# Performance work log

Measured on AMD Instinct MI355X. Metric: run time of the kernel, lower is better.

The kernel has to match this reference:

```python
import jax, jax.numpy as jnp
import numpy as np

H = 1024       # hidden_size
V = 32000      # output_vocab_size
STEPS = 375    # fixed greedy decode length in the original loop


def setup_inputs() -> dict:
    key = jax.random.key(0)
    ks = jax.random.split(key, 6)
    s = 0.02  # init scale
    return {
        "encoder_hidden": jax.random.normal(ks[0], (1, 1, H), dtype=jnp.float32),
        "emb": jax.random.normal(ks[1], (V, H), dtype=jnp.float32) * s,
        "W_ih": jax.random.normal(ks[2], (3 * H, H), dtype=jnp.float32) * s,   # [W_ir;W_iz;W_in]
        "W_hh": jax.random.normal(ks[3], (3 * H, H), dtype=jnp.float32) * s,   # [W_hr;W_hz;W_hn]
        "b_ih": jnp.zeros((3 * H,), dtype=jnp.float32),
        "b_hh": jnp.zeros((3 * H,), dtype=jnp.float32),
        "lin_W": jax.random.normal(ks[4], (V, H), dtype=jnp.float32) * s,
        "lin_b": jnp.zeros((V,), dtype=jnp.float32),
    }


def _gru_cell(x, h, W_ih, W_hh, b_ih, b_hh):
    # PyTorch GRU gate math (gate order r, z, n)
    gi = W_ih @ x + b_ih            # [3H]
    gh = W_hh @ h + b_hh            # [3H]
    i_r, i_z, i_n = jnp.split(gi, 3)
    h_r, h_z, h_n = jnp.split(gh, 3)
    r = jax.nn.sigmoid(i_r + h_r)
    z = jax.nn.sigmoid(i_z + h_z)
    n = jnp.tanh(i_n + r * h_n)
    return (1.0 - z) * n + z * h


def reference(encoder_hidden, emb, W_ih, W_hh, b_ih, b_hh, lin_W, lin_b):
    h0 = encoder_hidden[0, 0]  # [H], batch=1, single layer

    def step(carry, _):
        h, tok = carry
        x = emb[tok]                                   # embedding lookup [H]
        h_new = _gru_cell(x, h, W_ih, W_hh, b_ih, b_hh)
        logits = lin_W @ h_new + lin_b                 # [V]
        logp = jax.nn.log_softmax(logits)              # LogSoftmax(dim=1) on [1,V]
        next_tok = jnp.argmax(logp).astype(jnp.int32)  # greedy feedback
        return (h_new, next_tok), logp

    (h_final, _), outs = jax.lax.scan(
        step, (h0, jnp.int32(0)), None, length=STEPS)
    # original cats [1,V] outputs along dim 0 -> [STEPS, V]
    return outs, h_final.reshape(1, 1, H)
```

## Files before the change

### kernel.cpp

```cpp
#include <hip/hip_runtime.h>

#define H 1024
#define V 32000
#define STEPS 375
#define NB1 256
#define NB2 512
#define DELTA 0.0625f

__device__ __forceinline__ float dot4(const float4 a, const float4 b) {
    return fmaf(a.x, b.x, fmaf(a.y, b.y, fmaf(a.z, b.z, a.w * b.w)));
}

__device__ __forceinline__ float wave_sum(float v) {
#pragma unroll
    for (int off = 32; off > 0; off >>= 1) v += __shfl_xor(v, off);
    return v;
}

__device__ __forceinline__ void sm_merge(float& m, float& ss, int& a,
                                         float om, float os, int oa) {
    if (om > m || (om == m && oa < a)) {
        ss = os + ss * expf(m - om); m = om; a = oa;
    } else {
        ss += os * expf(om - m);
    }
}

__device__ __forceinline__ float bl(unsigned u) { return __uint_as_float(u << 16); }
__device__ __forceinline__ float bh(unsigned u) { return __uint_as_float(u & 0xffff0000u); }

__device__ __forceinline__ unsigned f2bf(float f) {
    unsigned u = __float_as_uint(f);
    return (u + 0x7fffu + ((u >> 16) & 1u)) >> 16;
}

__global__ void init_kernel(const float* __restrict__ enc, float* __restrict__ h0) {
    for (int i = threadIdx.x; i < H; i += 256) h0[i] = enc[i];
}

__global__ __launch_bounds__(512) void conv_kernel(const float* __restrict__ src,
                                                   unsigned short* __restrict__ dst) {
    const size_t idx = (size_t)blockIdx.x * 512 + threadIdx.x;
    const float4* s4 = (const float4*)src;
    float4 a = s4[2 * idx], b = s4[2 * idx + 1];
    uint4 o;
    o.x = f2bf(a.x) | (f2bf(a.y) << 16);
    o.y = f2bf(a.z) | (f2bf(a.w) << 16);
    o.z = f2bf(b.x) | (f2bf(b.y) << 16);
    o.w = f2bf(b.z) | (f2bf(b.w) << 16);
    ((uint4*)dst)[idx] = o;
}

__global__ __launch_bounds__(256) void gru_kernel(
    const float* __restrict__ emb, const float* __restrict__ W_ih,
    const float* __restrict__ W_hh, const float* __restrict__ b_ih,
    const float* __restrict__ b_hh, const float* __restrict__ h_cur,
    float* __restrict__ h_next, float* __restrict__ logz,
    const float* __restrict__ pm, const float* __restrict__ ps,
    const int* __restrict__ pa, int s) {
    const int tid = threadIdx.x;
    const int lane = tid & 63;
    const int wv = tid >> 6;
    const int b = blockIdx.x;
    const int i = b * 4 + wv;

    const float4* hp = (const float4*)h_cur;
    float4 hv[4];
    float4 WX0[4], WX1[4], WX2[4], WH0[4], WH1[4], WH2[4];
#pragma unroll
    for (int j = 0; j < 4; ++j) {
        const int idx = lane + 64 * j;
        hv[j] = hp[idx];
        WX0[j] = ((const float4*)(W_ih + (size_t)i * H))[idx];
        WX1[j] = ((const float4*)(W_ih + ((size_t)i + H) * H))[idx];
        WX2[j] = ((const float4*)(W_ih + ((size_t)i + 2 * H) * H))[idx];
        WH0[j] = ((const float4*)(W_hh + (size_t)i * H))[idx];
        WH1[j] = ((const float4*)(W_hh + ((size_t)i + H) * H))[idx];
        WH2[j] = ((const float4*)(W_hh + ((size_t)i + 2 * H) * H))[idx];
    }

    int tok = 0;
    if (s > 0) {
        float m = -3.4e38f, ss = 0.f;
        int a = 0x7fffffff;
#pragma unroll
        for (int k = 0; k < NB2 / 64; ++k)
            sm_merge(m, ss, a, pm[k * 64 + lane], ps[k * 64 + lane], pa[k * 64 + lane]);
#pragma unroll
        for (int off = 32; off > 0; off >>= 1) {
            float om = __shfl_xor(m, off), os = __shfl_xor(ss, off);
            int oa = __shfl_xor(a, off);
            sm_merge(m, ss, a, om, os, oa);
        }
        tok = a;
        if (b == 0 && tid == 0) logz[s - 1] = m + logf(ss);
    }

    const float4* xp = (const float4*)(emb + (size_t)tok * H);
    float4 xv[4];
#pragma unroll
    for (int j = 0; j < 4; ++j) xv[j] = xp[lane + 64 * j];

    float sx0 = 0, sx1 = 0, sx2 = 0, sh0 = 0, sh1 = 0, sh2 = 0;
#pragma unroll
    for (int j = 0; j < 4; ++j) {
        sx0 += dot4(WX0[j], xv[j]); sx1 += dot4(WX1[j], xv[j]); sx2 += dot4(WX2[j], xv[j]);
        sh0 += dot4(WH0[j], hv[j]); sh1 += dot4(WH1[j], hv[j]); sh2 += dot4(WH2[j], hv[j]);
    }
    sx0 = wave_sum(sx0); sx1 = wave_sum(sx1); sx2 = wave_sum(sx2);
    sh0 = wave_sum(sh0); sh1 = wave_sum(sh1); sh2 = wave_sum(sh2);
    if (lane == 0) {
        const float rg = 1.f / (1.f + expf(-((sx0 + b_ih[i]) + (sh0 + b_hh[i]))));
        const float zg = 1.f / (1.f + expf(-((sx1 + b_ih[i + H]) + (sh1 + b_hh[i + H]))));
        const float ng = tanhf((sx2 + b_ih[i + 2 * H]) + rg * (sh2 + b_hh[i + 2 * H]));
        h_next[i] = (1.f - zg) * ng + zg * h_cur[i];
    }
}

__global__ __launch_bounds__(512, 4) void logits_bf16_kernel(
    const unsigned short* __restrict__ wbf, const float* __restrict__ lin_W,
    const float* __restrict__ lin_b, const float* __restrict__ h_src,
    float* __restrict__ orow, float* __restrict__ pm, float* __restrict__ ps,
    int* __restrict__ pa) {
    const int tid = threadIdx.x;
    const int lane = tid & 63;
    const int wv = tid >> 6;
    const int b = blockIdx.x;
    const int row0 = (b < 256) ? 63 * b : 16128 + 62 * (b - 256);
    const int nrows = (b < 256) ? 63 : 62;

    __shared__ float red_m[8], red_s[8];
    __shared__ float s_cm[8];
    __shared__ int s_ca[8];

    const float4* h4 = (const float4*)h_src;
    const float4 ha0 = h4[2 * lane], ha1 = h4[2 * lane + 1];
    const float4 hb0 = h4[128 + 2 * lane], hb1 = h4[129 + 2 * lane];
    const float h0[8] = {ha0.x, ha0.y, ha0.z, ha0.w, ha1.x, ha1.y, ha1.z, ha1.w};
    const float h1[8] = {hb0.x, hb0.y, hb0.z, hb0.w, hb1.x, hb1.y, hb1.z, hb1.w};

    uint4 qa[8], qb[8];
    bool val[8];
#pragma unroll
    for (int k = 0; k < 8; ++k) {
        const int rr = wv + 8 * k;
        val[k] = rr < nrows;
        const uint4* wp = (const uint4*)(wbf + (size_t)(row0 + (val[k] ? rr : 0)) * H);
        qa[k] = wp[lane];
        qb[k] = wp[64 + lane];
    }
    __builtin_amdgcn_sched_barrier(0);

    float lg[8];
    float m = -3.4e38f, ssum = 0.f;
#pragma unroll
    for (int k = 0; k < 8; ++k) {
        float a = 0.f;
        a = fmaf(bl(qa[k].x), h0[0], a); a = fmaf(bh(qa[k].x), h0[1], a);
        a = fmaf(bl(qa[k].y), h0[2], a); a = fmaf(bh(qa[k].y), h0[3], a);
        a = fmaf(bl(qa[k].z), h0[4], a); a = fmaf(bh(qa[k].z), h0[5], a);
        a = fmaf(bl(qa[k].w), h0[6], a); a = fmaf(bh(qa[k].w), h0[7], a);
        a = fmaf(bl(qb[k].x), h1[0], a); a = fmaf(bh(qb[k].x), h1[1], a);
        a = fmaf(bl(qb[k].y), h1[2], a); a = fmaf(bh(qb[k].y), h1[3], a);
        a = fmaf(bl(qb[k].z), h1[4], a); a = fmaf(bh(qb[k].z), h1[5], a);
        a = fmaf(bl(qb[k].w), h1[6], a); a = fmaf(bh(qb[k].w), h1[7], a);
        a = wave_sum(a);
        if (val[k]) {
            const int col = row0 + wv + 8 * k;
            a += lin_b[col];
            lg[k] = a;
            if (lane == 0) __builtin_nontemporal_store(a, &orow[col]);
            if (a > m) { ssum *= expf(m - a); m = a; }
            ssum += expf(a - m);
        } else {
            lg[k] = -3.4e38f;
        }
    }
    if (lane == 0) { red_m[wv] = m; red_s[wv] = ssum; }
    __syncthreads();

    float Mb = red_m[0];
#pragma unroll
    for (int w = 1; w < 8; ++w) Mb = fmaxf(Mb, red_m[w]);

    float cm = -3.4e38f;
    int ca = 0x7fffffff;
    float4 hv[4];
    bool loaded = false;
#pragma unroll
    for (int k = 0; k < 8; ++k) {
        if (lg[k] > Mb - DELTA) {
            const int row = row0 + wv + 8 * k;
            if (!loaded) {
#pragma unroll
                for (int j = 0; j < 4; ++j) hv[j] = h4[lane + 64 * j];
                loaded = true;
            }
            const float4* rp = (const float4*)(lin_W + (size_t)row * H);
            float a = 0.f;
#pragma unroll
            for (int j = 0; j < 4; ++j) a += dot4(rp[lane + 64 * j], hv[j]);
            a = wave_sum(a) + lin_b[row];
            if (a > cm || (a == cm && row < ca)) { cm = a; ca = row; }
        }
    }
    if (lane == 0) { s_cm[wv] = cm; s_ca[wv] = ca; }
    __syncthreads();
    if (tid == 0) {
        float M = red_m[0], S = red_s[0];
#pragma unroll
        for (int w = 1; w < 8; ++w) {
            const float mw = red_m[w], sw = red_s[w];
            if (mw > M) { S = sw + S * expf(M - mw); M = mw; }
            else S += sw * expf(mw - M);
        }
        float CM = s_cm[0];
        int CA = s_ca[0];
#pragma unroll
        for (int w = 1; w < 8; ++w)
            if (s_cm[w] > CM || (s_cm[w] == CM && s_ca[w] < CA)) { CM = s_cm[w]; CA = s_ca[w]; }
        pm[b] = CM;
        ps[b] = S * expf(M - CM);
        pa[b] = CA;
    }
}

__global__ __launch_bounds__(512, 4) void logits_fp32_kernel(
    const float* __restrict__ lin_W, const float* __restrict__ lin_b,
    const float* __restrict__ h_src, float* __restrict__ orow,
    float* __restrict__ pm, float* __restrict__ ps, int* __restrict__ pa) {
    const int tid = threadIdx.x;
    const int lane = tid & 63;
    const int wv = tid >> 6;
    const int b = blockIdx.x;
    const int row0 = (b < 256) ? 63 * b : 16128 + 62 * (b - 256);
    const int nrows = (b < 256) ? 63 : 62;

    __shared__ float red_m[8], red_s[8];
    __shared__ int red_a[8];

    const float4* h4 = (const float4*)h_src;
    float4 hr[4];
#pragma unroll
    for (int j = 0; j < 4; ++j) hr[j] = h4[lane + 64 * j];

    float m = -3.4e38f, ssum = 0.f;
    int arg = 0x7fffffff;
    for (int r = wv; r < nrows; r += 32) {
        const int rB = r + 8, rC = r + 16, rD = r + 24;
        const bool vB = rB < nrows, vC = rC < nrows, vD = rD < nrows;
        float4 wA[4], wB[4], wC[4], wD[4];
#pragma unroll
        for (int j = 0; j < 4; ++j) {
            const int idx = lane + 64 * j;
            wA[j] = ((const float4*)(lin_W + (size_t)(row0 + r) * H))[idx];
            wB[j] = ((const float4*)(lin_W + (size_t)(row0 + (vB ? rB : r)) * H))[idx];
            wC[j] = ((const float4*)(lin_W + (size_t)(row0 + (vC ? rC : r)) * H))[idx];
            wD[j] = ((const float4*)(lin_W + (size_t)(row0 + (vD ? rD : r)) * H))[idx];
        }
        __builtin_amdgcn_sched_barrier(0);
        float aA = 0, aB = 0, aC = 0, aD = 0;
#pragma unroll
        for (int j = 0; j < 4; ++j) {
            aA += dot4(wA[j], hr[j]); aB += dot4(wB[j], hr[j]);
            aC += dot4(wC[j], hr[j]); aD += dot4(wD[j], hr[j]);
        }
        aA = wave_sum(aA); aB = wave_sum(aB);
        aC = wave_sum(aC); aD = wave_sum(aD);
        aA += lin_b[row0 + r];
        if (lane == 0) __builtin_nontemporal_store(aA, &orow[row0 + r]);
        if (aA > m) { ssum *= expf(m - aA); m = aA; arg = row0 + r; }
        ssum += expf(aA - m);
        if (vB) {
            aB += lin_b[row0 + rB];
            if (lane == 0) __builtin_nontemporal_store(aB, &orow[row0 + rB]);
            if (aB > m) { ssum *= expf(m - aB); m = aB; arg = row0 + rB; }
            ssum += expf(aB - m);
        }
        if (vC) {
            aC += lin_b[row0 + rC];
            if (lane == 0) __builtin_nontemporal_store(aC, &orow[row0 + rC]);
            if (aC > m) { ssum *= expf(m - aC); m = aC; arg = row0 + rC; }
            ssum += expf(aC - m);
        }
        if (vD) {
            aD += lin_b[row0 + rD];
            if (lane == 0) __builtin_nontemporal_store(aD, &orow[row0 + rD]);
            if (aD > m) { ssum *= expf(m - aD); m = aD; arg = row0 + rD; }
            ssum += expf(aD - m);
        }
    }
    if (lane == 0) { red_m[wv] = m; red_s[wv] = ssum; red_a[wv] = arg; }
    __syncthreads();
    if (tid == 0) {
        float M = red_m[0], S = red_s[0];
        int A = red_a[0];
#pragma unroll
        for (int w = 1; w < 8; ++w) sm_merge(M, S, A, red_m[w], red_s[w], red_a[w]);
        pm[b] = M; ps[b] = S; pa[b] = A;
    }
}

__global__ __launch_bounds__(256) void final_kernel(float* __restrict__ out,
                                                    const float* __restrict__ logz) {
    const int row = blockIdx.x >> 3;
    const int seg = blockIdx.x & 7;
    const float lz = logz[row];
    float4* p = (float4*)(out + (size_t)row * V) + seg * 1000;
    for (int i = threadIdx.x; i < 1000; i += 256) {
        float4 v = p[i];
        v.x -= lz; v.y -= lz; v.z -= lz; v.w -= lz;
        p[i] = v;
    }
}

__global__ __launch_bounds__(256) void tail_kernel(
    float* __restrict__ out_last, const float* __restrict__ pm,
    const float* __restrict__ ps, const int* __restrict__ pa,
    const float* __restrict__ h_final, float* __restrict__ out_h) {
    const int tid = threadIdx.x;
    const int lane = tid & 63;
    const int b = blockIdx.x;
    float m = -3.4e38f, ss = 0.f;
    int a = 0x7fffffff;
#pragma unroll
    for (int k = 0; k < NB2 / 64; ++k)
        sm_merge(m, ss, a, pm[k * 64 + lane], ps[k * 64 + lane], pa[k * 64 + lane]);
#pragma unroll
    for (int off = 32; off > 0; off >>= 1) {
        float om = __shfl_xor(m, off), os = __shfl_xor(ss, off);
        int oa = __shfl_xor(a, off);
        sm_merge(m, ss, a, om, os, oa);
    }
    const float logZ = m + logf(ss);
    if (tid < 125) out_last[b * 125 + tid] -= logZ;
    if (b == 0)
        for (int i = tid; i < H; i += 256) out_h[i] = h_final[i];
}

extern "C" void kernel_launch(void* const* d_in, const int* in_sizes, int n_in,
                              void* d_out, int out_size, void* d_ws, size_t ws_size,
                              hipStream_t stream) {
    const float* enc = (const float*)d_in[0];
    const float* emb = (const float*)d_in[1];
    const float* W_ih = (const float*)d_in[2];
    const float* W_hh = (const float*)d_in[3];
    const float* b_ih = (const float*)d_in[4];
    const float* b_hh = (const float*)d_in[5];
    const float* lin_W = (const float*)d_in[6];
    const float* lin_b = (const float*)d_in[7];
    float* out = (float*)d_out;
    float* ws = (float*)d_ws;

    float* h_buf = ws;
    float* pm = ws + 2 * H;
    float* ps = pm + NB2;
    int* pa = (int*)(ps + NB2);
    float* logz = (float*)(pa + NB2);
    unsigned short* wbf = (unsigned short*)((char*)d_ws + 16384);
    const size_t need = 16384 + (size_t)V * H * 2;
    const bool bf16path = ws_size >= need;

    init_kernel<<<1, 256, 0, stream>>>(enc, h_buf);
    if (bf16path)
        conv_kernel<<<V * H / 8 / 512, 512, 0, stream>>>(lin_W, wbf);
    for (int s = 0; s < STEPS; ++s) {
        float* h_cur = h_buf + (s & 1) * H;
        float* h_next = h_buf + ((s + 1) & 1) * H;
        gru_kernel<<<NB1, 256, 0, stream>>>(emb, W_ih, W_hh, b_ih, b_hh,
                                            h_cur, h_next, logz, pm, ps, pa, s);
        if (bf16path)
            logits_bf16_kernel<<<NB2, 512, 0, stream>>>(wbf, lin_W, lin_b, h_next,
                                                        out + (size_t)s * V, pm, ps, pa);
        else
            logits_fp32_kernel<<<NB2, 512, 0, stream>>>(lin_W, lin_b, h_next,
                                                        out + (size_t)s * V, pm, ps, pa);
    }
    final_kernel<<<(STEPS - 1) * 8, 256, 0, stream>>>(out, logz);
    tail_kernel<<<NB1, 256, 0, stream>>>(out + (size_t)(STEPS - 1) * V, pm, ps, pa,
                                         h_buf + (STEPS & 1) * H,
                                         out + (size_t)V * STEPS);
}
```

Before: 15.72 ms.

## Fuse log-softmax normalization into GRU kernel and restructure bf16 logits loads

The separate final pass that subtracted logZ from every stored logits row is removed. Each GRU launch now subtracts the previous step's logZ from its row while it has the reduced max and sum at hand, which avoids re-reading the whole output at the end. The GRU weight loads are moved after the token reduction, so register pressure during that reduction drops but load latency is no longer hidden behind it. The bf16 logits kernel now loads rows in two batches of four with a contiguous per-lane h layout, and reuses that h for the fp32 rescoring, lowering register use at the cost of less load overlap.

```diff
diff --git a/kernel.cpp b/kernel.cpp
--- a/kernel.cpp
+++ b/kernel.cpp
@@ -5,6 +5,7 @@
 #define STEPS 375
 #define NB1 256
 #define NB2 512
+#define RPB1 125
 #define DELTA 0.0625f
 
 __device__ __forceinline__ float dot4(const float4 a, const float4 b) {
@@ -55,29 +56,13 @@
     const float* __restrict__ emb, const float* __restrict__ W_ih,
     const float* __restrict__ W_hh, const float* __restrict__ b_ih,
     const float* __restrict__ b_hh, const float* __restrict__ h_cur,
-    float* __restrict__ h_next, float* __restrict__ logz,
+    float* __restrict__ h_next, float* __restrict__ out_prev,
     const float* __restrict__ pm, const float* __restrict__ ps,
     const int* __restrict__ pa, int s) {
     const int tid = threadIdx.x;
     const int lane = tid & 63;
     const int wv = tid >> 6;
     const int b = blockIdx.x;
-    const int i = b * 4 + wv;
-
-    const float4* hp = (const float4*)h_cur;
-    float4 hv[4];
-    float4 WX0[4], WX1[4], WX2[4], WH0[4], WH1[4], WH2[4];
-#pragma unroll
-    for (int j = 0; j < 4; ++j) {
-        const int idx = lane + 64 * j;
-        hv[j] = hp[idx];
-        WX0[j] = ((const float4*)(W_ih + (size_t)i * H))[idx];
-        WX1[j] = ((const float4*)(W_ih + ((size_t)i + H) * H))[idx];
-        WX2[j] = ((const float4*)(W_ih + ((size_t)i + 2 * H) * H))[idx];
-        WH0[j] = ((const float4*)(W_hh + (size_t)i * H))[idx];
-        WH1[j] = ((const float4*)(W_hh + ((size_t)i + H) * H))[idx];
-        WH2[j] = ((const float4*)(W_hh + ((size_t)i + 2 * H) * H))[idx];
-    }
 
     int tok = 0;
     if (s > 0) {
@@ -92,15 +77,33 @@
             int oa = __shfl_xor(a, off);
             sm_merge(m, ss, a, om, os, oa);
         }
+        const float logZ = m + logf(ss);
         tok = a;
-        if (b == 0 && tid == 0) logz[s - 1] = m + logf(ss);
-    }
-
+        if (tid < RPB1) out_prev[b * RPB1 + tid] -= logZ;
+    }
+
+    const int i = b * 4 + wv;
     const float4* xp = (const float4*)(emb + (size_t)tok * H);
-    float4 xv[4];
-#pragma unroll
-    for (int j = 0; j < 4; ++j) xv[j] = xp[lane + 64 * j];
-
+    const float4* hp = (const float4*)h_cur;
+    float4 xv[4], hv[4];
+#pragma unroll
+    for (int j = 0; j < 4; ++j) {
+        xv[j] = xp[lane + 64 * j];
+        hv[j] = hp[lane + 64 * j];
+    }
+    const float4* wx0 = (const float4*)(W_ih + (size_t)i * H);
+    const float4* wx1 = (const float4*)(W_ih + ((size_t)i + H) * H);
+    const float4* wx2 = (const float4*)(W_ih + ((size_t)i + 2 * H) * H);
+    const float4* wh0 = (const float4*)(W_hh + (size_t)i * H);
+    const float4* wh1 = (const float4*)(W_hh + ((size_t)i + H) * H);
+    const float4* wh2 = (const float4*)(W_hh + ((size_t)i + 2 * H) * H);
+    float4 WX0[4], WX1[4], WX2[4], WH0[4], WH1[4], WH2[4];
+#pragma unroll
+    for (int j = 0; j < 4; ++j) {
+        const int idx = lane + 64 * j;
+        WX0[j] = wx0[idx]; WX1[j] = wx1[idx]; WX2[j] = wx2[idx];
+        WH0[j] = wh0[idx]; WH1[j] = wh1[idx]; WH2[j] = wh2[idx];
+    }
     float sx0 = 0, sx1 = 0, sx2 = 0, sh0 = 0, sh1 = 0, sh2 = 0;
 #pragma unroll
     for (int j = 0; j < 4; ++j) {
@@ -134,46 +137,49 @@
     __shared__ int s_ca[8];
 
     const float4* h4 = (const float4*)h_src;
-    const float4 ha0 = h4[2 * lane], ha1 = h4[2 * lane + 1];
-    const float4 hb0 = h4[128 + 2 * lane], hb1 = h4[129 + 2 * lane];
-    const float h0[8] = {ha0.x, ha0.y, ha0.z, ha0.w, ha1.x, ha1.y, ha1.z, ha1.w};
-    const float h1[8] = {hb0.x, hb0.y, hb0.z, hb0.w, hb1.x, hb1.y, hb1.z, hb1.w};
-
-    uint4 qa[8], qb[8];
-    bool val[8];
-#pragma unroll
-    for (int k = 0; k < 8; ++k) {
-        const int rr = wv + 8 * k;
-        val[k] = rr < nrows;
-        const uint4* wp = (const uint4*)(wbf + (size_t)(row0 + (val[k] ? rr : 0)) * H);
-        qa[k] = wp[lane];
-        qb[k] = wp[64 + lane];
-    }
-    __builtin_amdgcn_sched_barrier(0);
+    float4 hv[4];
+#pragma unroll
+    for (int j = 0; j < 4; ++j) hv[j] = h4[4 * lane + j];
 
     float lg[8];
     float m = -3.4e38f, ssum = 0.f;
-#pragma unroll
-    for (int k = 0; k < 8; ++k) {
-        float a = 0.f;
-        a = fmaf(bl(qa[k].x), h0[0], a); a = fmaf(bh(qa[k].x), h0[1], a);
-        a = fmaf(bl(qa[k].y), h0[2], a); a = fmaf(bh(qa[k].y), h0[3], a);
-        a = fmaf(bl(qa[k].z), h0[4], a); a = fmaf(bh(qa[k].z), h0[5], a);
-        a = fmaf(bl(qa[k].w), h0[6], a); a = fmaf(bh(qa[k].w), h0[7], a);
-        a = fmaf(bl(qb[k].x), h1[0], a); a = fmaf(bh(qb[k].x), h1[1], a);
-        a = fmaf(bl(qb[k].y), h1[2], a); a = fmaf(bh(qb[k].y), h1[3], a);
-        a = fmaf(bl(qb[k].z), h1[4], a); a = fmaf(bh(qb[k].z), h1[5], a);
-        a = fmaf(bl(qb[k].w), h1[6], a); a = fmaf(bh(qb[k].w), h1[7], a);
-        a = wave_sum(a);
-        if (val[k]) {
-            const int col = row0 + wv + 8 * k;
-            a += lin_b[col];
-            lg[k] = a;
-            if (lane == 0) __builtin_nontemporal_store(a, &orow[col]);
-            if (a > m) { ssum *= expf(m - a); m = a; }
-            ssum += expf(a - m);
-        } else {
-            lg[k] = -3.4e38f;
+
+#pragma unroll
+    for (int it = 0; it < 2; ++it) {
+        uint4 q[4][2];
+        bool val[4];
+#pragma unroll
+        for (int kq = 0; kq < 4; ++kq) {
+            const int rr = wv + 8 * (4 * it + kq);
+            val[kq] = rr < nrows;
+            const uint4* wp = (const uint4*)(wbf + (size_t)(row0 + (val[kq] ? rr : 0)) * H);
+            q[kq][0] = wp[2 * lane];
+            q[kq][1] = wp[2 * lane + 1];
+        }
+        __builtin_amdgcn_sched_barrier(0);
+#pragma unroll
+        for (int kq = 0; kq < 4; ++kq) {
+            const int slot = 4 * it + kq;
+            float a = 0.f;
+            a = fmaf(bl(q[kq][0].x), hv[0].x, a); a = fmaf(bh(q[kq][0].x), hv[0].y, a);
+            a = fmaf(bl(q[kq][0].y), hv[0].z, a); a = fmaf(bh(q[kq][0].y), hv[0].w, a);
+            a = fmaf(bl(q[kq][0].z), hv[1].x, a); a = fmaf(bh(q[kq][0].z), hv[1].y, a);
+            a = fmaf(bl(q[kq][0].w), hv[1].z, a); a = fmaf(bh(q[kq][0].w), hv[1].w, a);
+            a = fmaf(bl(q[kq][1].x), hv[2].x, a); a = fmaf(bh(q[kq][1].x), hv[2].y, a);
+            a = fmaf(bl(q[kq][1].y), hv[2].z, a); a = fmaf(bh(q[kq][1].y), hv[2].w, a);
+            a = fmaf(bl(q[kq][1].z), hv[3].x, a); a = fmaf(bh(q[kq][1].z), hv[3].y, a);
+            a = fmaf(bl(q[kq][1].w), hv[3].z, a); a = fmaf(bh(q[kq][1].w), hv[3].w, a);
+            a = wave_sum(a);
+            if (val[kq]) {
+                const int col = row0 + wv + 8 * slot;
+                a += lin_b[col];
+                lg[slot] = a;
+                if (lane == 0) __builtin_nontemporal_store(a, &orow[col]);
+                if (a > m) { ssum *= expf(m - a); m = a; }
+                ssum += expf(a - m);
+            } else {
+                lg[slot] = -3.4e38f;
+            }
         }
     }
     if (lane == 0) { red_m[wv] = m; red_s[wv] = ssum; }
@@ -185,21 +191,14 @@
 
     float cm = -3.4e38f;
     int ca = 0x7fffffff;
-    float4 hv[4];
-    bool loaded = false;
 #pragma unroll
     for (int k = 0; k < 8; ++k) {
         if (lg[k] > Mb - DELTA) {
             const int row = row0 + wv + 8 * k;
-            if (!loaded) {
-#pragma unroll
-                for (int j = 0; j < 4; ++j) hv[j] = h4[lane + 64 * j];
-                loaded = true;
-            }
             const float4* rp = (const float4*)(lin_W + (size_t)row * H);
             float a = 0.f;
 #pragma unroll
-            for (int j = 0; j < 4; ++j) a += dot4(rp[lane + 64 * j], hv[j]);
+            for (int j = 0; j < 4; ++j) a += dot4(rp[4 * lane + j], hv[j]);
             a = wave_sum(a) + lin_b[row];
             if (a > cm || (a == cm && row < ca)) { cm = a; ca = row; }
         }
@@ -301,19 +300,6 @@
     }
 }
 
-__global__ __launch_bounds__(256) void final_kernel(float* __restrict__ out,
-                                                    const float* __restrict__ logz) {
-    const int row = blockIdx.x >> 3;
-    const int seg = blockIdx.x & 7;
-    const float lz = logz[row];
-    float4* p = (float4*)(out + (size_t)row * V) + seg * 1000;
-    for (int i = threadIdx.x; i < 1000; i += 256) {
-        float4 v = p[i];
-        v.x -= lz; v.y -= lz; v.z -= lz; v.w -= lz;
-        p[i] = v;
-    }
-}
-
 __global__ __launch_bounds__(256) void tail_kernel(
     float* __restrict__ out_last, const float* __restrict__ pm,
     const float* __restrict__ ps, const int* __restrict__ pa,
@@ -333,7 +319,7 @@
         sm_merge(m, ss, a, om, os, oa);
     }
     const float logZ = m + logf(ss);
-    if (tid < 125) out_last[b * 125 + tid] -= logZ;
+    if (tid < RPB1) out_last[b * RPB1 + tid] -= logZ;
     if (b == 0)
         for (int i = tid; i < H; i += 256) out_h[i] = h_final[i];
 }
@@ -356,7 +342,6 @@
     float* pm = ws + 2 * H;
     float* ps = pm + NB2;
     int* pa = (int*)(ps + NB2);
-    float* logz = (float*)(pa + NB2);
     unsigned short* wbf = (unsigned short*)((char*)d_ws + 16384);
     const size_t need = 16384 + (size_t)V * H * 2;
     const bool bf16path = ws_size >= need;
@@ -367,8 +352,10 @@
     for (int s = 0; s < STEPS; ++s) {
         float* h_cur = h_buf + (s & 1) * H;
         float* h_next = h_buf + ((s + 1) & 1) * H;
+        float* out_prev = out + (size_t)(s > 0 ? s - 1 : 0) * V;
         gru_kernel<<<NB1, 256, 0, stream>>>(emb, W_ih, W_hh, b_ih, b_hh,
-                                            h_cur, h_next, logz, pm, ps, pa, s);
+                                            h_cur, h_next, out_prev,
+                                            pm, ps, pa, s);
         if (bf16path)
             logits_bf16_kernel<<<NB2, 512, 0, stream>>>(wbf, lin_W, lin_b, h_next,
                                                         out + (size_t)s * V, pm, ps, pa);
@@ -376,7 +363,6 @@
             logits_fp32_kernel<<<NB2, 512, 0, stream>>>(lin_W, lin_b, h_next,
                                                         out + (size_t)s * V, pm, ps, pa);
     }
-    final_kernel<<<(STEPS - 1) * 8, 256, 0, stream>>>(out, logz);
     tail_kernel<<<NB1, 256, 0, stream>>>(out + (size_t)(STEPS - 1) * V, pm, ps, pa,
                                          h_buf + (STEPS & 1) * H,
                                          out + (size_t)V * STEPS);
```

After: 15.67 ms. Within noise of the previous version (-0.3%).
